# Performance work log

Measured on AMD Instinct MI355X. Metric: run time of the kernel, lower is better.

## Reference

```python
import jax, jax.numpy as jnp
import numpy as np

B, S, H, NH = 1, 2048, 1024, 16
HD = H // NH
LAYER_NUMBER = 1
EPS = 1e-5
NEG_INF = -1e9


def _layernorm(x, g, b):
    mu = jnp.mean(x, axis=-1, keepdims=True)
    var = jnp.mean((x - mu) ** 2, axis=-1, keepdims=True)
    return (x - mu) * jax.lax.rsqrt(var + EPS) * g + b


def _bloom_gelu(x):
    # tanh approximation used by Megatron/Bloom
    return x * 0.5 * (1.0 + jnp.tanh(0.79788456 * x * (1.0 + 0.044715 * x * x)))


def setup_inputs() -> dict:
    key = jax.random.key(0)
    ks = jax.random.split(key, 8)

    def w(k, shape, scale=0.02):
        return jax.random.normal(k, shape, jnp.float32) * scale

    # additive causal mask: 0 where attended, -1e9 where masked
    causal = jnp.where(jnp.tril(jnp.ones((S, S), bool)), 0.0, NEG_INF).astype(jnp.float32)
    attention_mask = causal[None, None]  # [1,1,S,S]

    return {
        "hidden_states": jax.random.normal(ks[0], (B, S, H), jnp.float32),
        "attention_mask": attention_mask,
        "alibi": w(ks[1], (B * NH, 1, S), 1.0),
        "ln1_g": jnp.ones((H,), jnp.float32),
        "ln1_b": jnp.zeros((H,), jnp.float32),
        "qkv_w": w(ks[2], (3 * H, H)),
        "qkv_b": jnp.zeros((3 * H,), jnp.float32),
        "dense_w": w(ks[3], (H, H)),
        "dense_b": jnp.zeros((H,), jnp.float32),
        "ln2_g": jnp.ones((H,), jnp.float32),
        "ln2_b": jnp.zeros((H,), jnp.float32),
        "fc1_w": w(ks[4], (4 * H, H)),
        "fc1_b": jnp.zeros((4 * H,), jnp.float32),
        "fc2_w": w(ks[5], (H, 4 * H)),
        "fc2_b": jnp.zeros((H,), jnp.float32),
    }


def reference(hidden_states, attention_mask, alibi,
              ln1_g, ln1_b, qkv_w, qkv_b, dense_w, dense_b,
              ln2_g, ln2_b, fc1_w, fc1_b, fc2_w, fc2_b):
    dtype = hidden_states.dtype
    norm_factor = np.sqrt(HD).astype(np.float32) * LAYER_NUMBER
    beta = 1.0 / LAYER_NUMBER

    # --- input layernorm (residual = pre-LN hidden states) ---
    ln_out = _layernorm(hidden_states, ln1_g, ln1_b)
    residual = hidden_states

    # --- attention ---
    fused = ln_out @ qkv_w.T + qkv_b                      # [B,S,3H]
    fused = fused.reshape(B, S, NH, 3 * HD)
    q, k, v = fused[..., :HD], fused[..., HD:2 * HD], fused[..., 2 * HD:]

    scores = jnp.einsum('bqhd,bkhd->bhqk', q, k) / norm_factor \
             + beta * alibi.reshape(B, NH, 1, S)          # [B,NH,S,S]
    attn = scores * LAYER_NUMBER + attention_mask
    attn = jnp.maximum(attn, jnp.finfo(attn.dtype).min)
    probs = jax.nn.softmax(attn.astype(jnp.float32), axis=-1).astype(dtype)
    probs = probs * (attention_mask == 0.0)               # zero out masked positions

    ctx = jnp.einsum('bhqk,bkhd->bqhd', probs, v).reshape(B, S, H)
    attn_out = ctx @ dense_w.T + dense_b + residual       # dropout_add, p=0

    # --- post-attention layernorm + MLP ---
    ln2_out = _layernorm(attn_out, ln2_g, ln2_b)
    residual2 = attn_out
    h = _bloom_gelu(ln2_out @ fc1_w.T + fc1_b)            # [B,S,4H]
    out = h @ fc2_w.T + fc2_b + residual2                 # dropout_add, p=0
    return out
```

## Files before the change

kernel.cpp:

```cpp
#include <hip/hip_runtime.h>
#include <hip/hip_bf16.h>

typedef unsigned short u16;
typedef __attribute__((ext_vector_type(8))) short bf16x8;
typedef __attribute__((ext_vector_type(4))) float f32x4;

typedef __attribute__((address_space(1))) const void cgvoid;
typedef __attribute__((address_space(3))) void lvoid;

static __device__ __forceinline__ u16 f2bf(float x) {
    __hip_bfloat16 h = __float2bfloat16(x);
    return __builtin_bit_cast(u16, h);
}

static __device__ __forceinline__ void gload_lds16(const u16* g, u16* l) {
    __builtin_amdgcn_global_load_lds((cgvoid*)g, (lvoid*)l, 16, 0, 0);
}

__global__ __launch_bounds__(256) void prep(
    const float* __restrict__ hidden, const float* __restrict__ g1,
    const float* __restrict__ b1, u16* __restrict__ ln_out,
    const float* __restrict__ qkv_w, const float* __restrict__ dense_w,
    const float* __restrict__ fc1_w, const float* __restrict__ fc2_w,
    u16* __restrict__ qkv_wb, u16* __restrict__ dense_wb,
    u16* __restrict__ fc1_wb, u16* __restrict__ fc2_wb)
{
    const int t = threadIdx.x;
    if (blockIdx.x < 2048) {
        const int row = blockIdx.x;
        const float4 v = ((const float4*)(hidden + (size_t)row * 1024))[t];
        float s  = v.x + v.y + v.z + v.w;
        float sq = v.x*v.x + v.y*v.y + v.z*v.z + v.w*v.w;
#pragma unroll
        for (int d = 1; d < 64; d <<= 1) {
            s  += __shfl_xor(s, d, 64);
            sq += __shfl_xor(sq, d, 64);
        }
        __shared__ float ss[4], ssq[4];
        const int wave = t >> 6, lane = t & 63;
        if (lane == 0) { ss[wave] = s; ssq[wave] = sq; }
        __syncthreads();
        s  = ss[0] + ss[1] + ss[2] + ss[3];
        sq = ssq[0] + ssq[1] + ssq[2] + ssq[3];
        const float mu = s * (1.f / 1024.f);
        const float rinv = rsqrtf(sq * (1.f / 1024.f) - mu * mu + 1e-5f);
        const float4 gv = ((const float4*)g1)[t];
        const float4 bv = ((const float4*)b1)[t];
        ushort4 pk;
        pk.x = f2bf((v.x - mu) * rinv * gv.x + bv.x);
        pk.y = f2bf((v.y - mu) * rinv * gv.y + bv.y);
        pk.z = f2bf((v.z - mu) * rinv * gv.z + bv.z);
        pk.w = f2bf((v.w - mu) * rinv * gv.w + bv.w);
        ((ushort4*)(ln_out + (size_t)row * 1024))[t] = pk;
        return;
    }
    constexpr int C0 = 786432;
    constexpr int C1 = C0 + 262144;
    constexpr int C2 = C1 + 1048576;
    constexpr int C3 = C2 + 1048576;
    int i = (blockIdx.x - 2048) * 256 + t;
    const int stride = (gridDim.x - 2048) * 256;
    for (; i < C3; i += stride) {
        const float* src; u16* dst; int j;
        if (i < C0)      { src = qkv_w;   dst = qkv_wb;   j = i; }
        else if (i < C1) { src = dense_w; dst = dense_wb; j = i - C0; }
        else if (i < C2) { src = fc1_w;   dst = fc1_wb;   j = i - C1; }
        else             { src = fc2_w;   dst = fc2_wb;   j = i - C2; }
        const float4 v = ((const float4*)src)[j];
        ushort4 pk;
        pk.x = f2bf(v.x); pk.y = f2bf(v.y); pk.z = f2bf(v.z); pk.w = f2bf(v.w);
        ((ushort4*)dst)[j] = pk;
    }
}

template<int EPI, int BN>
__global__ __launch_bounds__(256, 4) void gemm_bt(
    const u16* __restrict__ A, const u16* __restrict__ Bw,
    const float* __restrict__ bias, void* __restrict__ Cout,
    float* __restrict__ p0, float* __restrict__ pext,
    int M, int N, int K, int Kspan)
{
    constexpr int WC = BN / 64;
    constexpr int MI = (BN == 128) ? 4 : 2;
    constexpr int NI = 4;
    __shared__ __align__(16) u16 As[128 * 64];
    __shared__ __align__(16) u16 Bs[BN * 64];
    const int t = threadIdx.x;
    const int lane = t & 63;
    const int wave = t >> 6;
    const int wr = wave / WC, wc = wave % WC;
    const int g = lane >> 4, r16 = lane & 15;

    const int nxy = gridDim.x * gridDim.y;
    int bid = blockIdx.x + gridDim.x * blockIdx.y;
    const int v = (bid & 7) * (nxy >> 3) + (bid >> 3);
    const int tile_m = (v / gridDim.y) * 128;
    const int tile_n = (v % gridDim.y) * BN;
    const int kb = blockIdx.z * Kspan;

    f32x4 acc[MI][NI] = {};

    for (int k0 = kb; k0 < kb + Kspan; k0 += 64) {
        __syncthreads();
#pragma unroll
        for (int i = 0; i < 4; ++i) {
            const int off = (t + i * 256) * 8;
            gload_lds16(A + (size_t)(tile_m + (off >> 6)) * K + k0 + (off & 63), As + off);
        }
#pragma unroll
        for (int i = 0; i < BN / 32; ++i) {
            const int off = (t + i * 256) * 8;
            gload_lds16(Bw + (size_t)(tile_n + (off >> 6)) * K + k0 + (off & 63), Bs + off);
        }
        __syncthreads();

        bf16x8 af[MI][2], bfr[NI][2];
#pragma unroll
        for (int mi = 0; mi < MI; ++mi)
#pragma unroll
            for (int ks = 0; ks < 2; ++ks)
                af[mi][ks] = *(const bf16x8*)(As + (wr*(MI*16) + mi*16 + r16)*64 + ks*32 + g*8);
#pragma unroll
        for (int ni = 0; ni < NI; ++ni)
#pragma unroll
            for (int ks = 0; ks < 2; ++ks)
                bfr[ni][ks] = *(const bf16x8*)(Bs + (wc*64 + ni*16 + r16)*64 + ks*32 + g*8);
#pragma unroll
        for (int mi = 0; mi < MI; ++mi)
#pragma unroll
            for (int ni = 0; ni < NI; ++ni) {
                acc[mi][ni] = __builtin_amdgcn_mfma_f32_16x16x32_bf16(af[mi][0], bfr[ni][0], acc[mi][ni], 0, 0, 0);
                acc[mi][ni] = __builtin_amdgcn_mfma_f32_16x16x32_bf16(af[mi][1], bfr[ni][1], acc[mi][ni], 0, 0, 0);
            }
    }

    float* dst = nullptr;
    if constexpr (EPI == 4)
        dst = (blockIdx.z == 0) ? p0 : pext + (size_t)(blockIdx.z - 1) * ((size_t)M * N);

#pragma unroll
    for (int mi = 0; mi < MI; ++mi) {
#pragma unroll
        for (int ni = 0; ni < NI; ++ni) {
            const int col = tile_n + wc*64 + ni*16 + r16;
            const int row0 = tile_m + wr*(MI*16) + mi*16 + g*4;
#pragma unroll
            for (int r = 0; r < 4; ++r) {
                const int row = row0 + r;
                if constexpr (EPI == 4) {
                    dst[(size_t)row * N + col] = acc[mi][ni][r];
                } else if constexpr (EPI == 0) {
                    ((u16*)Cout)[(size_t)row * N + col] = f2bf(acc[mi][ni][r] + bias[col]);
                } else {
                    const float v2 = acc[mi][ni][r] + bias[col];
                    const float c = 0.79788456f * v2 * (1.0f + 0.044715f * v2 * v2);
                    ((u16*)Cout)[(size_t)row * N + col] = f2bf(v2 / (1.0f + __expf(-2.0f * c)));
                }
            }
        }
    }
}

__global__ __launch_bounds__(256) void reduce2_ln(
    const float* __restrict__ p0, const float* __restrict__ p1,
    const float* __restrict__ bias, const float* __restrict__ res,
    float* __restrict__ attn_o, const float* __restrict__ g2,
    const float* __restrict__ b2, u16* __restrict__ ln_out)
{
    const int row = blockIdx.x;
    const int t = threadIdx.x;
    const size_t i = (size_t)row * 256 + t;
    const float4 a0 = ((const float4*)p0)[i];
    const float4 a1 = ((const float4*)p1)[i];
    const float4 bv = ((const float4*)bias)[t];
    const float4 rv = ((const float4*)res)[i];
    float4 v;
    v.x = a0.x + a1.x + bv.x + rv.x;
    v.y = a0.y + a1.y + bv.y + rv.y;
    v.z = a0.z + a1.z + bv.z + rv.z;
    v.w = a0.w + a1.w + bv.w + rv.w;
    ((float4*)attn_o)[i] = v;

    float s  = v.x + v.y + v.z + v.w;
    float sq = v.x*v.x + v.y*v.y + v.z*v.z + v.w*v.w;
#pragma unroll
    for (int d = 1; d < 64; d <<= 1) {
        s  += __shfl_xor(s, d, 64);
        sq += __shfl_xor(sq, d, 64);
    }
    __shared__ float ss[4], ssq[4];
    const int wave = t >> 6, lane = t & 63;
    if (lane == 0) { ss[wave] = s; ssq[wave] = sq; }
    __syncthreads();
    s  = ss[0] + ss[1] + ss[2] + ss[3];
    sq = ssq[0] + ssq[1] + ssq[2] + ssq[3];
    const float mu = s * (1.f / 1024.f);
    const float rinv = rsqrtf(sq * (1.f / 1024.f) - mu * mu + 1e-5f);
    const float4 gv = ((const float4*)g2)[t];
    const float4 b2v = ((const float4*)b2)[t];
    ushort4 pk;
    pk.x = f2bf((v.x - mu) * rinv * gv.x + b2v.x);
    pk.y = f2bf((v.y - mu) * rinv * gv.y + b2v.y);
    pk.z = f2bf((v.z - mu) * rinv * gv.z + b2v.z);
    pk.w = f2bf((v.w - mu) * rinv * gv.w + b2v.w);
    ((ushort4*)(ln_out + (size_t)row * 1024))[t] = pk;
}

template<int NP>
__global__ __launch_bounds__(256) void reduce_bias_res(
    const float* __restrict__ p0, const float* __restrict__ pext,
    const float* __restrict__ bias, const float* __restrict__ res,
    float* __restrict__ out, int n4, int n4row)
{
    int i = blockIdx.x * blockDim.x + threadIdx.x;
    const int stride = gridDim.x * blockDim.x;
    for (; i < n4; i += stride) {
        float4 a = ((const float4*)p0)[i];
#pragma unroll
        for (int j = 0; j < NP - 1; ++j) {
            const float4 b = ((const float4*)pext)[(size_t)j * n4 + i];
            a.x += b.x; a.y += b.y; a.z += b.z; a.w += b.w;
        }
        const float4 bv = ((const float4*)bias)[i & (n4row - 1)];
        const float4 rv = ((const float4*)res)[i];
        float4 o;
        o.x = a.x + bv.x + rv.x;
        o.y = a.y + bv.y + rv.y;
        o.z = a.z + bv.z + rv.z;
        o.w = a.w + bv.w + rv.w;
        ((float4*)out)[i] = o;
    }
}

__global__ __launch_bounds__(256) void pack_kv(
    const u16* __restrict__ fused, u16* __restrict__ kP, u16* __restrict__ vP)
{
    const int bid = blockIdx.x;
    const int h = bid >> 5, kt = bid & 31;
    const int kt0 = kt * 64;
    const int t = threadIdx.x;
    const int lane = t & 63;
    const int g = lane >> 4, r16 = lane & 15;
    const size_t tbase = ((size_t)(h * 32 + kt)) * 4096;

#pragma unroll
    for (int half = 0; half < 2; ++half) {
        const int gi = (t >> 6) + half * 4;
        const int kn = gi >> 1, ks = gi & 1;
        const int w = 32*(kn>>1) + 8*(r16>>2) + 4*(kn&1) + (r16&3);
        const bf16x8 kv = *(const bf16x8*)(fused + (size_t)(kt0 + w) * 3072 + h*192 + 64 + ks*32 + g*8);
        *(bf16x8*)(kP + tbase + gi*512 + lane*8) = kv;
        union { bf16x8 v; u16 e[8]; } uv;
        const u16* vs = fused + (size_t)(kt0 + ks*32 + g*8) * 3072 + h*192 + 128 + kn*16 + r16;
#pragma unroll
        for (int e = 0; e < 8; ++e) uv.e[e] = vs[(size_t)e * 3072];
        *(bf16x8*)(vP + tbase + gi*512 + lane*8) = uv.v;
    }
}

__global__ __launch_bounds__(256, 4) void attn_swapped(
    const u16* __restrict__ fused, const u16* __restrict__ kP,
    const u16* __restrict__ vP, const float* __restrict__ alibi,
    u16* __restrict__ ctx)
{
    const int bid = blockIdx.x;
    const int h = bid & 15;
    const int qt = 127 - (bid >> 4);
    const int qw0 = qt * 16;
    const int t = threadIdx.x;
    const int lane = t & 63, wave = t >> 6;
    const int g = lane >> 4, r16 = lane & 15;
    const int qrow = qw0 + r16;

    __shared__ float Ms[4][16], Ls[4][16];
    __shared__ float Os[4][4][16][17];

    const u16* qbase = fused + (size_t)qrow * 3072 + h * 192;
    bf16x8 qf[2];
    qf[0] = *(const bf16x8*)(qbase + g*8);
    qf[1] = *(const bf16x8*)(qbase + 32 + g*8);

    f32x4 o_acc[4] = {};
    float m_r = -3.0e38f, l_r = 0.f;

    const u16* kPh = kP + (size_t)h * 32 * 4096;
    const u16* vPh = vP + (size_t)h * 32 * 4096;
    const float* abase = alibi + (size_t)h * 2048;

    const int nkt = (qw0 >> 6) + 1;
    for (int kt = wave; kt < nkt; kt += 4) {
        const int kt0 = kt * 64;
        const u16* kT = kPh + (size_t)kt * 4096;
        const u16* vT = vPh + (size_t)kt * 4096;

        bf16x8 kf[4][2], vf[4][2];
#pragma unroll
        for (int kn = 0; kn < 4; ++kn) {
            kf[kn][0] = *(const bf16x8*)(kT + (kn*2 + 0)*512 + lane*8);
            kf[kn][1] = *(const bf16x8*)(kT + (kn*2 + 1)*512 + lane*8);
        }
        float4 al[4];
#pragma unroll
        for (int kn = 0; kn < 4; ++kn)
            al[kn] = *(const float4*)(abase + kt0 + 32*(kn>>1) + 8*g + 4*(kn&1));
#pragma unroll
        for (int nd = 0; nd < 4; ++nd) {
            vf[nd][0] = *(const bf16x8*)(vT + (nd*2 + 0)*512 + lane*8);
            vf[nd][1] = *(const bf16x8*)(vT + (nd*2 + 1)*512 + lane*8);
        }

        f32x4 sc[4] = {};
#pragma unroll
        for (int kn = 0; kn < 4; ++kn) {
            sc[kn] = __builtin_amdgcn_mfma_f32_16x16x32_bf16(kf[kn][0], qf[0], sc[kn], 0, 0, 0);
            sc[kn] = __builtin_amdgcn_mfma_f32_16x16x32_bf16(kf[kn][1], qf[1], sc[kn], 0, 0, 0);
        }

        float s[4][4];
        float rmax = -3.0e38f;
#pragma unroll
        for (int kn = 0; kn < 4; ++kn) {
            const int kb = kt0 + 32*(kn>>1) + 8*g + 4*(kn&1);
            const float alv[4] = {al[kn].x, al[kn].y, al[kn].z, al[kn].w};
#pragma unroll
            for (int r = 0; r < 4; ++r) {
                float v = sc[kn][r] * 0.125f + alv[r];
                v = (kb + r <= qrow) ? v : -1.0e30f;
                s[kn][r] = v;
                rmax = fmaxf(rmax, v);
            }
        }
        rmax = fmaxf(rmax, __shfl_xor(rmax, 16, 64));
        rmax = fmaxf(rmax, __shfl_xor(rmax, 32, 64));

        const float mnew = fmaxf(m_r, rmax);
        const float scale = __expf(m_r - mnew);
        m_r = mnew;

        float psum = 0.f;
        u16 ph[4][4];
#pragma unroll
        for (int kn = 0; kn < 4; ++kn)
#pragma unroll
            for (int r = 0; r < 4; ++r) {
                const float p = __expf(s[kn][r] - mnew);
                psum += p;
                ph[kn][r] = f2bf(p);
            }
        psum += __shfl_xor(psum, 16, 64);
        psum += __shfl_xor(psum, 32, 64);
        l_r = l_r * scale + psum;

#pragma unroll
        for (int nd = 0; nd < 4; ++nd)
#pragma unroll
            for (int r = 0; r < 4; ++r)
                o_acc[nd][r] *= scale;

        bf16x8 pf[2];
#pragma unroll
        for (int ks = 0; ks < 2; ++ks) {
            union { bf16x8 v; u16 e[8]; } u;
#pragma unroll
            for (int r = 0; r < 4; ++r) { u.e[r] = ph[2*ks][r]; u.e[4+r] = ph[2*ks+1][r]; }
            pf[ks] = u.v;
        }
#pragma unroll
        for (int nd = 0; nd < 4; ++nd) {
            o_acc[nd] = __builtin_amdgcn_mfma_f32_16x16x32_bf16(vf[nd][0], pf[0], o_acc[nd], 0, 0, 0);
            o_acc[nd] = __builtin_amdgcn_mfma_f32_16x16x32_bf16(vf[nd][1], pf[1], o_acc[nd], 0, 0, 0);
        }
    }

#pragma unroll
    for (int nd = 0; nd < 4; ++nd)
#pragma unroll
        for (int r = 0; r < 4; ++r)
            Os[wave][nd][g*4 + r][r16] = o_acc[nd][r];
    if (g == 0) { Ms[wave][r16] = m_r; Ls[wave][r16] = l_r; }
    __syncthreads();

    if (wave == 0) {
        const float m0 = Ms[0][r16], m1 = Ms[1][r16], m2 = Ms[2][r16], m3 = Ms[3][r16];
        const float ms = fmaxf(fmaxf(m0, m1), fmaxf(m2, m3));
        const float f0 = __expf(m0 - ms), f1 = __expf(m1 - ms);
        const float f2 = __expf(m2 - ms), f3 = __expf(m3 - ms);
        const float l = f0*Ls[0][r16] + f1*Ls[1][r16] + f2*Ls[2][r16] + f3*Ls[3][r16];
        const float inv = 1.0f / l;
#pragma unroll
        for (int nd = 0; nd < 4; ++nd) {
            float v[4];
#pragma unroll
            for (int r = 0; r < 4; ++r) {
                const int d = g*4 + r;
                v[r] = (f0*Os[0][nd][d][r16] + f1*Os[1][nd][d][r16] +
                        f2*Os[2][nd][d][r16] + f3*Os[3][nd][d][r16]) * inv;
            }
            ushort4 pk;
            pk.x = f2bf(v[0]); pk.y = f2bf(v[1]); pk.z = f2bf(v[2]); pk.w = f2bf(v[3]);
            *(ushort4*)(ctx + (size_t)qrow * 1024 + h*64 + nd*16 + g*4) = pk;
        }
    }
}

extern "C" void kernel_launch(void* const* d_in, const int* in_sizes, int n_in,
                              void* d_out, int out_size, void* d_ws, size_t ws_size,
                              hipStream_t stream)
{
    (void)in_sizes; (void)n_in; (void)out_size; (void)ws_size;
    const float* hidden  = (const float*)d_in[0];
    const float* alibi   = (const float*)d_in[2];
    const float* ln1_g   = (const float*)d_in[3];
    const float* ln1_b   = (const float*)d_in[4];
    const float* qkv_w   = (const float*)d_in[5];
    const float* qkv_b   = (const float*)d_in[6];
    const float* dense_w = (const float*)d_in[7];
    const float* dense_b = (const float*)d_in[8];
    const float* ln2_g   = (const float*)d_in[9];
    const float* ln2_b   = (const float*)d_in[10];
    const float* fc1_w   = (const float*)d_in[11];
    const float* fc1_b   = (const float*)d_in[12];
    const float* fc2_w   = (const float*)d_in[13];
    const float* fc2_b   = (const float*)d_in[14];
    float* out = (float*)d_out;

    char* p = (char*)d_ws;
    u16* ln_buf   = (u16*)p;  p += (size_t)2048 * 1024 * 2;
    u16* qkv_wb   = (u16*)p;  p += (size_t)3072 * 1024 * 2;
    u16* fusedq   = (u16*)p;  p += (size_t)2048 * 3072 * 2;
    u16* ctx      = (u16*)p;  p += (size_t)2048 * 1024 * 2;
    u16* dense_wb = (u16*)p;  p += (size_t)1024 * 1024 * 2;
    float* attn_o = (float*)p; p += (size_t)2048 * 1024 * 4;
    u16* fc1_wb   = (u16*)p;  p += (size_t)4096 * 1024 * 2;
    u16* fc2_wb   = (u16*)p;  p += (size_t)1024 * 4096 * 2;
    float* pext   = (float*)p; p += (size_t)3 * 2048 * 1024 * 4;
    float* part0  = (float*)p; p += (size_t)2048 * 1024 * 4;
    u16* hbuf = fusedq;
    u16* kP = (u16*)attn_o;
    u16* vP = kP + (size_t)16 * 32 * 4096;

    prep<<<6144, 256, 0, stream>>>(hidden, ln1_g, ln1_b, ln_buf,
                                   qkv_w, dense_w, fc1_w, fc2_w,
                                   qkv_wb, dense_wb, fc1_wb, fc2_wb);
    gemm_bt<0,64><<<dim3(16, 48), 256, 0, stream>>>(ln_buf, qkv_wb, qkv_b, fusedq,
                                                    nullptr, nullptr, 2048, 3072, 1024, 1024);
    pack_kv<<<512, 256, 0, stream>>>(fusedq, kP, vP);
    attn_swapped<<<2048, 256, 0, stream>>>(fusedq, kP, vP, alibi, ctx);
    gemm_bt<4,64><<<dim3(16, 16, 2), 256, 0, stream>>>(ctx, dense_wb, nullptr, nullptr,
                                                       part0, pext, 2048, 1024, 1024, 512);
    reduce2_ln<<<2048, 256, 0, stream>>>(part0, pext, dense_b, hidden, attn_o,
                                         ln2_g, ln2_b, ln_buf);
    gemm_bt<2,64><<<dim3(16, 64), 256, 0, stream>>>(ln_buf, fc1_wb, fc1_b, hbuf,
                                                    nullptr, nullptr, 2048, 4096, 1024, 1024);
    gemm_bt<4,64><<<dim3(16, 16, 4), 256, 0, stream>>>(hbuf, fc2_wb, nullptr, nullptr,
                                                       part0, pext, 2048, 1024, 4096, 1024);
    reduce_bias_res<4><<<2048, 256, 0, stream>>>(part0, pext, fc2_b, attn_o, out,
                                                 2048*1024/4, 256);
}
```

Measured before the change: 167.2 us.

## Fuse K/V packing into QKV GEMM epilogue and widen GEMM N-tiles

The QKV GEMM epilogue now writes K and V directly into the packed per-head tile layouts the attention kernel expects, so the separate pack_kv kernel and its re-read of the fused buffer are dropped. The QKV, FC1 and FC2 GEMMs switch from 64-wide to 128-wide N tiles, with launch bounds relaxed from 4 to 2 blocks per SM. The aim is fewer launches, less memory traffic and more operand reuse per tile. The cost is scattered, partly scalar stores in the epilogue, possibly lower occupancy, and fewer blocks per grid.

```diff
diff --git a/kernel.cpp b/kernel.cpp
--- a/kernel.cpp
+++ b/kernel.cpp
@@ -74,10 +74,11 @@
 }
 
 template<int EPI, int BN>
-__global__ __launch_bounds__(256, 4) void gemm_bt(
+__global__ __launch_bounds__(256, 2) void gemm_bt(
     const u16* __restrict__ A, const u16* __restrict__ Bw,
     const float* __restrict__ bias, void* __restrict__ Cout,
     float* __restrict__ p0, float* __restrict__ pext,
+    u16* __restrict__ kPo, u16* __restrict__ vPo,
     int M, int N, int K, int Kspan)
 {
     constexpr int WC = BN / 64;
@@ -92,8 +93,8 @@
     const int g = lane >> 4, r16 = lane & 15;
 
     const int nxy = gridDim.x * gridDim.y;
-    int bid = blockIdx.x + gridDim.x * blockIdx.y;
-    const int v = (bid & 7) * (nxy >> 3) + (bid >> 3);
+    const int bid0 = blockIdx.x + gridDim.x * blockIdx.y;
+    const int v = (bid0 & 7) * (nxy >> 3) + (bid0 >> 3);
     const int tile_m = (v / gridDim.y) * 128;
     const int tile_n = (v % gridDim.y) * BN;
     const int kb = blockIdx.z * Kspan;
@@ -144,17 +145,47 @@
         for (int ni = 0; ni < NI; ++ni) {
             const int col = tile_n + wc*64 + ni*16 + r16;
             const int row0 = tile_m + wr*(MI*16) + mi*16 + g*4;
+            float vv[4];
+#pragma unroll
+            for (int r = 0; r < 4; ++r) {
+                if constexpr (EPI == 4) vv[r] = acc[mi][ni][r];
+                else                    vv[r] = acc[mi][ni][r] + bias[col];
+            }
 #pragma unroll
             for (int r = 0; r < 4; ++r) {
                 const int row = row0 + r;
                 if constexpr (EPI == 4) {
-                    dst[(size_t)row * N + col] = acc[mi][ni][r];
-                } else if constexpr (EPI == 0) {
-                    ((u16*)Cout)[(size_t)row * N + col] = f2bf(acc[mi][ni][r] + bias[col]);
+                    dst[(size_t)row * N + col] = vv[r];
+                } else if constexpr (EPI == 0 || EPI == 3) {
+                    ((u16*)Cout)[(size_t)row * N + col] = f2bf(vv[r]);
                 } else {
-                    const float v2 = acc[mi][ni][r] + bias[col];
-                    const float c = 0.79788456f * v2 * (1.0f + 0.044715f * v2 * v2);
-                    ((u16*)Cout)[(size_t)row * N + col] = f2bf(v2 / (1.0f + __expf(-2.0f * c)));
+                    const float c = 0.79788456f * vv[r] * (1.0f + 0.044715f * vv[r] * vv[r]);
+                    ((u16*)Cout)[(size_t)row * N + col] = f2bf(vv[r] / (1.0f + __expf(-2.0f * c)));
+                }
+            }
+            if constexpr (EPI == 3) {
+                const int h = col / 192;
+                const int fm = col % 192;
+                if ((fm >> 6) == 1) {
+                    const int f = fm - 64;
+                    const int ks = f >> 5, gg = (f >> 3) & 3, e = f & 7;
+#pragma unroll
+                    for (int r = 0; r < 4; ++r) {
+                        const int tkn = row0 + r;
+                        const int kt = tkn >> 6, w = tkn & 63;
+                        const int kn = ((w >> 5) << 1) | ((w >> 2) & 1);
+                        const int rp = ((w >> 3) & 3) * 4 + (w & 3);
+                        kPo[((size_t)(h*32 + kt))*4096 + (kn*2 + ks)*512 + (gg*16 + rp)*8 + e] = f2bf(vv[r]);
+                    }
+                } else if ((fm >> 6) == 2) {
+                    const int f = fm - 128;
+                    const int nd = f >> 4, rv = f & 15;
+                    const int kt = row0 >> 6, w = row0 & 63;
+                    const int ks = w >> 5, gg = (w >> 3) & 3, e0 = w & 7;
+                    ushort4 pk4;
+                    pk4.x = f2bf(vv[0]); pk4.y = f2bf(vv[1]);
+                    pk4.z = f2bf(vv[2]); pk4.w = f2bf(vv[3]);
+                    *(ushort4*)(vPo + ((size_t)(h*32 + kt))*4096 + (nd*2 + ks)*512 + (gg*16 + rv)*8 + e0) = pk4;
                 }
             }
         }
@@ -232,32 +263,6 @@
     }
 }
 
-__global__ __launch_bounds__(256) void pack_kv(
-    const u16* __restrict__ fused, u16* __restrict__ kP, u16* __restrict__ vP)
-{
-    const int bid = blockIdx.x;
-    const int h = bid >> 5, kt = bid & 31;
-    const int kt0 = kt * 64;
-    const int t = threadIdx.x;
-    const int lane = t & 63;
-    const int g = lane >> 4, r16 = lane & 15;
-    const size_t tbase = ((size_t)(h * 32 + kt)) * 4096;
-
-#pragma unroll
-    for (int half = 0; half < 2; ++half) {
-        const int gi = (t >> 6) + half * 4;
-        const int kn = gi >> 1, ks = gi & 1;
-        const int w = 32*(kn>>1) + 8*(r16>>2) + 4*(kn&1) + (r16&3);
-        const bf16x8 kv = *(const bf16x8*)(fused + (size_t)(kt0 + w) * 3072 + h*192 + 64 + ks*32 + g*8);
-        *(bf16x8*)(kP + tbase + gi*512 + lane*8) = kv;
-        union { bf16x8 v; u16 e[8]; } uv;
-        const u16* vs = fused + (size_t)(kt0 + ks*32 + g*8) * 3072 + h*192 + 128 + kn*16 + r16;
-#pragma unroll
-        for (int e = 0; e < 8; ++e) uv.e[e] = vs[(size_t)e * 3072];
-        *(bf16x8*)(vP + tbase + gi*512 + lane*8) = uv.v;
-    }
-}
-
 __global__ __launch_bounds__(256, 4) void attn_swapped(
     const u16* __restrict__ fused, const u16* __restrict__ kP,
     const u16* __restrict__ vP, const float* __restrict__ alibi,
@@ -442,18 +447,21 @@
     prep<<<6144, 256, 0, stream>>>(hidden, ln1_g, ln1_b, ln_buf,
                                    qkv_w, dense_w, fc1_w, fc2_w,
                                    qkv_wb, dense_wb, fc1_wb, fc2_wb);
-    gemm_bt<0,64><<<dim3(16, 48), 256, 0, stream>>>(ln_buf, qkv_wb, qkv_b, fusedq,
-                                                    nullptr, nullptr, 2048, 3072, 1024, 1024);
-    pack_kv<<<512, 256, 0, stream>>>(fusedq, kP, vP);
+    gemm_bt<3,128><<<dim3(16, 24), 256, 0, stream>>>(ln_buf, qkv_wb, qkv_b, fusedq,
+                                                     nullptr, nullptr, kP, vP,
+                                                     2048, 3072, 1024, 1024);
     attn_swapped<<<2048, 256, 0, stream>>>(fusedq, kP, vP, alibi, ctx);
     gemm_bt<4,64><<<dim3(16, 16, 2), 256, 0, stream>>>(ctx, dense_wb, nullptr, nullptr,
-                                                       part0, pext, 2048, 1024, 1024, 512);
+                                                       part0, pext, nullptr, nullptr,
+                                                       2048, 1024, 1024, 512);
     reduce2_ln<<<2048, 256, 0, stream>>>(part0, pext, dense_b, hidden, attn_o,
                                          ln2_g, ln2_b, ln_buf);
-    gemm_bt<2,64><<<dim3(16, 64), 256, 0, stream>>>(ln_buf, fc1_wb, fc1_b, hbuf,
-                                                    nullptr, nullptr, 2048, 4096, 1024, 1024);
-    gemm_bt<4,64><<<dim3(16, 16, 4), 256, 0, stream>>>(hbuf, fc2_wb, nullptr, nullptr,
-                                                       part0, pext, 2048, 1024, 4096, 1024);
+    gemm_bt<2,128><<<dim3(16, 32), 256, 0, stream>>>(ln_buf, fc1_wb, fc1_b, hbuf,
+                                                     nullptr, nullptr, nullptr, nullptr,
+                                                     2048, 4096, 1024, 1024);
+    gemm_bt<4,128><<<dim3(16, 8, 4), 256, 0, stream>>>(hbuf, fc2_wb, nullptr, nullptr,
+                                                       part0, pext, nullptr, nullptr,
+                                                       2048, 1024, 4096, 1024);
     reduce_bias_res<4><<<2048, 256, 0, stream>>>(part0, pext, fc2_b, attn_o, out,
                                                  2048*1024/4, 256);
 }
```

After: 163.9 us. 2.0% less time.
